# Kernel tuning notes

Hardware: AMD Instinct MI355X
Metric: run time of the kernel (lower is better)

The kernel has to match this reference:

```python
import jax, jax.numpy as jnp
import numpy as np

B, N, DIN, DOUT, DOP = 64, 512, 256, 256, 64
LN_EPS = 1e-5
NEG_SLOPE = 0.2


def setup_inputs() -> dict:
    key = jax.random.key(0)
    ks = jax.random.split(key, 16)
    stdv = 1.0 / np.sqrt(DOUT)

    def lin(k, shape, fan_in):
        # torch nn.Linear default init: U(-1/sqrt(fan_in), 1/sqrt(fan_in))
        bound = 1.0 / np.sqrt(fan_in)
        return jax.random.uniform(k, shape, jnp.float32, -bound, bound)

    return {
        "inputs": jax.random.normal(ks[0], (B, N, DIN), jnp.float32),
        "adj": jax.random.uniform(ks[1], (B, N, N), jnp.float32),
        "op_emb": jax.random.normal(ks[2], (B, N, DOP), jnp.float32),
        # DenseGraphFlow params
        "dgf_W": jax.random.uniform(ks[3], (DIN, DOUT), jnp.float32, -stdv, stdv),
        "dgf_b": jax.random.uniform(ks[4], (DOUT,), jnp.float32, -stdv, stdv),
        "dgf_opW": lin(ks[5], (DOUT, DOP), DOP),
        "dgf_opb": lin(ks[6], (DOUT,), DOP),
        # GraphAttentionLayer params
        "Wk": lin(ks[7], (DOUT, DIN), DIN),
        "Wv": lin(ks[8], (DOUT, DIN), DIN),
        "Wq": lin(ks[9], (DOUT, DIN), DIN),
        "a_w": lin(ks[10], (DOUT,), DOUT),
        "gat_opW": lin(ks[11], (DOUT, DOP), DOP),
        "gat_opb": lin(ks[12], (DOUT,), DOP),
        "ln_g": jnp.ones((DOUT,), jnp.float32),
        "ln_b": jnp.zeros((DOUT,), jnp.float32),
    }


def reference(inputs, adj, op_emb, dgf_W, dgf_b, dgf_opW, dgf_opb,
              Wk, Wv, Wq, a_w, gat_opW, gat_opb, ln_g, ln_b):
    # ----- DenseGraphFlow branch -----
    support = jnp.einsum('bni,io->bno', inputs, dgf_W)            # [B,N,DOUT]
    gate_d = jax.nn.sigmoid(op_emb @ dgf_opW.T + dgf_opb)        # [B,N,DOUT]
    dense = gate_d * jnp.einsum('bij,bjo->bio', adj, support)
    dense = dense + support + dgf_b                               # residual + bias

    # ----- GraphAttentionLayer branch -----
    Whk = inputs @ Wk.T                                           # [B,N,DOUT]
    Whv = inputs @ Wv.T
    Whq = inputs @ Wq.T
    # torch einsum 'balm,beam->belm' (a=1) builds Whq[b,e,:]*Whk[b,l,:];
    # a(.) contracts the feature dim -> equivalent fused score:
    scores = jnp.einsum('bem,blm,m->bel', Whq, Whk, a_w)
    scores = scores / jnp.sqrt(jnp.float32(DOUT))                 # attention_rescale
    alpha = jax.nn.leaky_relu(scores, NEG_SLOPE) * adj            # mask by multiply
    attn = jax.nn.softmax(alpha, axis=-1)                         # softmax over l (neighbors)
    gate_g = jax.nn.sigmoid(op_emb @ gat_opW.T + gat_opb)
    h_prime = gate_g * jnp.einsum('bel,blm->bem', attn, Whv)
    # LayerNorm over last dim
    mu = jnp.mean(h_prime, axis=-1, keepdims=True)
    var = jnp.var(h_prime, axis=-1, keepdims=True)
    gat = (h_prime - mu) * jax.lax.rsqrt(var + LN_EPS) * ln_g + ln_b

    return (dense + gat) * 0.5
```

## Files before the change

kernel.cpp:

```cpp
#include <hip/hip_runtime.h>
#include <cstdint>
#include <cstddef>

typedef unsigned short u16;
typedef unsigned int   u32;
typedef __attribute__((ext_vector_type(8))) short bf16x8;
typedef __attribute__((ext_vector_type(4))) float f32x4;

#define MFMA16(a,b,c) __builtin_amdgcn_mfma_f32_16x16x32_bf16((a),(b),(c),0,0,0)

__device__ __forceinline__ float bf2f(u16 h){
  union { u32 u; float f; } v; v.u = ((u32)h) << 16; return v.f;
}
__device__ __forceinline__ u16 f2bf(float f){
  union { float f; u32 u; } v; v.f = f;
  u32 u = v.u + 0x7FFFu + ((v.u >> 16) & 1u);
  return (u16)(u >> 16);
}
__device__ __forceinline__ float ldf(const void* p, int i, u32 isf32){
  return isf32 ? ((const float*)p)[i] : bf2f(((const u16*)p)[i]);
}
__device__ __forceinline__ void gld16(const u16* g, u16* l){
  __builtin_amdgcn_global_load_lds(
      (const __attribute__((address_space(1))) void*)g,
      (__attribute__((address_space(3))) void*)l, 16, 0, 0);
}

__global__ void kD_detect(const u16* __restrict__ raw, u32* __restrict__ flag)
{
  const int lane = threadIdx.x & 63;
  const float v = bf2f(raw[lane]);
  const unsigned long long big = __ballot(fabsf(v) > 1.0e6f);
  if (lane == 0) flag[0] = (big != 0ull) ? 1u : 0u;
}

__global__ void kC_conv(const void* __restrict__ src, u16* __restrict__ dst,
                        int n, const u32* __restrict__ flag)
{
  const int i8 = (blockIdx.x * 256 + threadIdx.x) << 3;
  if (i8 >= n) return;
  if (flag[0]) {
    const float4 a = ((const float4*)src)[i8 >> 2];
    const float4 b = ((const float4*)src)[(i8 >> 2) + 1];
    u16 o[8] = { f2bf(a.x), f2bf(a.y), f2bf(a.z), f2bf(a.w),
                 f2bf(b.x), f2bf(b.y), f2bf(b.z), f2bf(b.w) };
    *(uint4*)&dst[i8] = *(const uint4*)o;
  } else {
    ((uint4*)dst)[i8 >> 3] = ((const uint4*)src)[i8 >> 3];
  }
}

__global__ void kP_params(const void* dgf_opW, const void* gat_opW,
                          const void* dgf_b,   const void* dgf_opb,
                          const void* gat_opb, const void* ln_g,
                          const void* ln_b,    u16* __restrict__ PB,
                          const u32* __restrict__ flag)
{
  const int i = blockIdx.x * 256 + threadIdx.x;
  if (i >= 34048) return;
  const u32 f = flag[0];
  float v;
  if      (i < 16384) v = ldf(dgf_opW, i, f);
  else if (i < 32768) v = ldf(gat_opW, i - 16384, f);
  else if (i < 33024) v = ldf(dgf_b,   i - 32768, f);
  else if (i < 33280) v = ldf(dgf_opb, i - 33024, f);
  else if (i < 33536) v = ldf(gat_opb, i - 33280, f);
  else if (i < 33792) v = ldf(ln_g,    i - 33536, f);
  else                v = ldf(ln_b,    i - 33792, f);
  PB[i] = f2bf(v);
}

__global__ void k0_wcat(const void* dgfW, const void* Wk, const void* Wv,
                        const void* Wq, const void* aw, u16* __restrict__ Wcat,
                        const u32* __restrict__ flag)
{
  const int o = blockIdx.x;
  const int i = threadIdx.x;
  const u32 f = flag[0];
  float v;
  if (o < 256)       v = ldf(dgfW, i * 256 + o, f);
  else if (o < 512)  v = ldf(Wk, (o - 256) * 256 + i, f);
  else if (o < 768)  v = ldf(Wv, (o - 512) * 256 + i, f);
  else               v = ldf(Wq, (o - 768) * 256 + i, f) * ldf(aw, o - 768, f) * 0.0625f;
  Wcat[o * 256 + i] = f2bf(v);
}

__global__ __launch_bounds__(256, 2)
void k1_proj(const u16* __restrict__ X, const u16* __restrict__ W,
             u16* __restrict__ P, u16* __restrict__ T)
{
  __shared__ __align__(16) u16 ldsA[128 * 64];
  __shared__ __align__(16) u16 ldsB[128 * 64];
  const int bt = blockIdx.x;
  const int ct = blockIdx.y;
  const int r0 = bt << 7;
  const bool swapped = (ct == 4) | (ct == 5) | (ct >= 8);
  const int wbase = (ct < 8) ? (ct << 7) : ((ct - 8) << 7);
  const int tid = threadIdx.x;
  const int wave = tid >> 6;
  const int lane = tid & 63;
  const int wm = wave >> 1, wn = wave & 1;

  int gA[4], gB[4], dS[4];
#pragma unroll
  for (int s = 0; s < 4; ++s) {
    const int slot = ((wave * 4 + s) << 6) + lane;
    const int m = slot >> 3, c = slot & 7;
    const int kb = c ^ (m & 7);
    gA[s] = (r0 + m) * 256 + (kb << 3);
    gB[s] = (wbase + m) * 256 + (kb << 3);
    dS[s] = slot << 3;
  }

  f32x4 acc[4][4];
#pragma unroll
  for (int i = 0; i < 4; ++i)
#pragma unroll
    for (int j = 0; j < 4; ++j) acc[i][j] = f32x4{0.f, 0.f, 0.f, 0.f};

  for (int kt = 0; kt < 4; ++kt) {
    __syncthreads();
#pragma unroll
    for (int s = 0; s < 4; ++s) {
      gld16(X + gA[s] + (kt << 6), &ldsA[dS[s]]);
      gld16(W + gB[s] + (kt << 6), &ldsB[dS[s]]);
    }
    __syncthreads();
#pragma unroll
    for (int ks = 0; ks < 2; ++ks) {
      const int kb = (ks << 2) + (lane >> 4);
      bf16x8 fa[4], fb[4];
#pragma unroll
      for (int i = 0; i < 4; ++i) {
        const int m = (wm << 6) + (i << 4) + (lane & 15);
        fa[i] = *(const bf16x8*)&ldsA[((m << 3) + (kb ^ (m & 7))) << 3];
        const int n = (wn << 6) + (i << 4) + (lane & 15);
        fb[i] = *(const bf16x8*)&ldsB[((n << 3) + (kb ^ (n & 7))) << 3];
      }
      if (!swapped) {
#pragma unroll
        for (int i = 0; i < 4; ++i)
#pragma unroll
          for (int j = 0; j < 4; ++j)
            acc[i][j] = MFMA16(fa[i], fb[j], acc[i][j]);
      } else {
#pragma unroll
        for (int i = 0; i < 4; ++i)
#pragma unroll
          for (int j = 0; j < 4; ++j)
            acc[i][j] = MFMA16(fb[i], fa[j], acc[i][j]);
      }
    }
  }

  if (!swapped) {
    const int pcb = (ct < 4) ? (ct << 7) : ((ct - 2) << 7);
#pragma unroll
    for (int i = 0; i < 4; ++i) {
      const int row = r0 + (wm << 6) + (i << 4) + ((lane >> 4) << 2);
#pragma unroll
      for (int j = 0; j < 4; ++j) {
        const int col = pcb + (wn << 6) + (j << 4) + (lane & 15);
#pragma unroll
        for (int r = 0; r < 4; ++r)
          P[(row + r) * 768 + col] = f2bf(acc[i][j][r]);
      }
    }
  } else {
    const int trb = (wbase >= 512) ? (wbase - 256) : wbase;
    const int b = r0 >> 9;
    const int e0 = r0 & 511;
    u16* Tb = T + ((size_t)b << 18);
#pragma unroll
    for (int i = 0; i < 4; ++i) {
      const int trow = trb + (wn << 6) + (i << 4) + ((lane >> 4) << 2);
#pragma unroll
      for (int j = 0; j < 4; ++j) {
        const int e = e0 + (wm << 6) + (j << 4) + (lane & 15);
#pragma unroll
        for (int r = 0; r < 4; ++r)
          Tb[((trow + r) << 9) + e] = f2bf(acc[i][j][r]);
      }
    }
  }
}

__global__ __launch_bounds__(256, 2)
void k2_gates(const u16* __restrict__ OP, const u16* __restrict__ PB,
              u16* __restrict__ G)
{
  __shared__ __align__(16) u16 ldsA[128 * 64];
  __shared__ __align__(16) u16 ldsB[128 * 64];
  const int bt = blockIdx.x, ct = blockIdx.y;
  const int r0 = bt << 7;
  const u16* Wp = (ct < 2) ? (PB + (ct << 7) * 64) : (PB + 16384 + ((ct - 2) << 7) * 64);
  const u16* Bp = (ct < 2) ? (PB + 33024 + (ct << 7)) : (PB + 33280 + ((ct - 2) << 7));
  const int tid = threadIdx.x, wave = tid >> 6, lane = tid & 63;
  const int wm = wave >> 1, wn = wave & 1;

  f32x4 acc[4][4];
#pragma unroll
  for (int i = 0; i < 4; ++i)
#pragma unroll
    for (int j = 0; j < 4; ++j) acc[i][j] = f32x4{0.f, 0.f, 0.f, 0.f};

#pragma unroll
  for (int s = 0; s < 4; ++s) {
    const int slot = ((wave * 4 + s) << 6) + lane;
    const int m = slot >> 3, c = slot & 7;
    const int kb = c ^ (m & 7);
    *(uint4*)&ldsA[slot << 3] = *(const uint4*)(OP + (r0 + m) * 64 + (kb << 3));
    *(uint4*)&ldsB[slot << 3] = *(const uint4*)(Wp + m * 64 + (kb << 3));
  }
  __syncthreads();
#pragma unroll
  for (int ks = 0; ks < 2; ++ks) {
    const int kb = (ks << 2) + (lane >> 4);
    bf16x8 fa[4], fb[4];
#pragma unroll
    for (int i = 0; i < 4; ++i) {
      const int m = (wm << 6) + (i << 4) + (lane & 15);
      fa[i] = *(const bf16x8*)&ldsA[((m << 3) + (kb ^ (m & 7))) << 3];
      const int n = (wn << 6) + (i << 4) + (lane & 15);
      fb[i] = *(const bf16x8*)&ldsB[((n << 3) + (kb ^ (n & 7))) << 3];
    }
#pragma unroll
    for (int i = 0; i < 4; ++i)
#pragma unroll
      for (int j = 0; j < 4; ++j)
        acc[i][j] = MFMA16(fa[i], fb[j], acc[i][j]);
  }
#pragma unroll
  for (int i = 0; i < 4; ++i) {
    const int row = r0 + (wm << 6) + (i << 4) + ((lane >> 4) << 2);
#pragma unroll
    for (int j = 0; j < 4; ++j) {
      const int cw = (wn << 6) + (j << 4) + (lane & 15);
      const float bias = bf2f(Bp[cw]);
      const int col = (ct << 7) + cw;
#pragma unroll
      for (int r = 0; r < 4; ++r) {
        const float x = acc[i][j][r] + bias;
        G[((row + r) << 9) + col] = f2bf(1.0f / (1.0f + __expf(-x)));
      }
    }
  }
}

__global__ __launch_bounds__(256, 2)
void k3_scores(const u16* __restrict__ P, const u16* __restrict__ adj,
               u16* __restrict__ E)
{
  __shared__ __align__(16) u16 ldsA[128 * 64];
  __shared__ __align__(16) u16 ldsB[128 * 64];
  const int lt = blockIdx.x, et = blockIdx.y, b = blockIdx.z;
  const int e0 = et << 7, l0 = lt << 7;
  const int tid = threadIdx.x, wave = tid >> 6, lane = tid & 63;
  const int wm = wave >> 1, wn = wave & 1;
  const int rowQ = (b << 9) + e0;
  const int rowK = (b << 9) + l0;

  int gA[4], gB[4], dS[4];
#pragma unroll
  for (int s = 0; s < 4; ++s) {
    const int slot = ((wave * 4 + s) << 6) + lane;
    const int m = slot >> 3, c = slot & 7;
    const int kb = c ^ (m & 7);
    gA[s] = (rowQ + m) * 768 + 512 + (kb << 3);
    gB[s] = (rowK + m) * 768 + 256 + (kb << 3);
    dS[s] = slot << 3;
  }

  f32x4 acc[4][4];
#pragma unroll
  for (int i = 0; i < 4; ++i)
#pragma unroll
    for (int j = 0; j < 4; ++j) acc[i][j] = f32x4{0.f, 0.f, 0.f, 0.f};

  for (int kt = 0; kt < 4; ++kt) {
    __syncthreads();
#pragma unroll
    for (int s = 0; s < 4; ++s) {
      gld16(P + gA[s] + (kt << 6), &ldsA[dS[s]]);
      gld16(P + gB[s] + (kt << 6), &ldsB[dS[s]]);
    }
    __syncthreads();
#pragma unroll
    for (int ks = 0; ks < 2; ++ks) {
      const int kb = (ks << 2) + (lane >> 4);
      bf16x8 fa[4], fb[4];
#pragma unroll
      for (int i = 0; i < 4; ++i) {
        const int m = (wm << 6) + (i << 4) + (lane & 15);
        fa[i] = *(const bf16x8*)&ldsA[((m << 3) + (kb ^ (m & 7))) << 3];
        const int n = (wn << 6) + (i << 4) + (lane & 15);
        fb[i] = *(const bf16x8*)&ldsB[((n << 3) + (kb ^ (n & 7))) << 3];
      }
#pragma unroll
      for (int i = 0; i < 4; ++i)
#pragma unroll
        for (int j = 0; j < 4; ++j)
          acc[i][j] = MFMA16(fa[i], fb[j], acc[i][j]);
    }
  }
#pragma unroll
  for (int i = 0; i < 4; ++i) {
    const int e = e0 + (wm << 6) + (i << 4) + ((lane >> 4) << 2);
#pragma unroll
    for (int j = 0; j < 4; ++j) {
      const int l = l0 + (wn << 6) + (j << 4) + (lane & 15);
#pragma unroll
      for (int r = 0; r < 4; ++r) {
        const int idx = (((b << 9) + e + r) << 9) + l;
        const float a = bf2f(adj[idx]);
        float s = acc[i][j][r];
        s = (s > 0.0f ? s : 0.2f * s) * a;
        E[idx] = f2bf(__expf(s));
      }
    }
  }
}

__global__ __launch_bounds__(256, 2)
void k4_out(const u16* __restrict__ P, const u16* __restrict__ T,
            const u16* __restrict__ E, const u16* __restrict__ adj,
            const u16* __restrict__ G, const u16* __restrict__ PB,
            void* __restrict__ out, const u32* __restrict__ flag)
{
  __shared__ __align__(16) u16 ldsA[64 * 64];
  __shared__ __align__(16) u16 ldsB[256 * 64];
  __shared__ float red[64][4];
  const int et = blockIdx.x, b = blockIdx.y;
  const int e0 = et << 6;
  const int tid = threadIdx.x, wave = tid >> 6, lane = tid & 63;
  const int wm = wave >> 1, wn = wave & 1;
  const size_t abase = ((size_t)((b << 9) + e0)) << 9;
  const u16* Ea  = E + abase;
  const u16* Aa  = adj + abase;
  const u16* Tb  = T + ((size_t)b << 18);
  const u16* WhvT = Tb + (256 << 9);
  const u16* SupT = Tb;
  const u16* dgf_b = PB + 32768;
  const u16* ln_g  = PB + 33536;
  const u16* ln_b  = PB + 33792;
  const u32 isf32 = flag[0];

  int gA[2], dA[2], gB[8], dB[8];
#pragma unroll
  for (int s2 = 0; s2 < 2; ++s2) {
    const int slot = ((wave * 2 + s2) << 6) + lane;
    const int m = slot >> 3, c = slot & 7;
    gA[s2] = (m << 9) + ((c ^ (m & 7)) << 3);
    dA[s2] = slot << 3;
  }
#pragma unroll
  for (int s2 = 0; s2 < 8; ++s2) {
    const int slot = ((wave * 8 + s2) << 6) + lane;
    const int m = slot >> 3, c = slot & 7;
    gB[s2] = (m << 9) + ((c ^ (m & 7)) << 3);
    dB[s2] = slot << 3;
  }

  f32x4 acc[2][2][8], accS[2];
#pragma unroll
  for (int i = 0; i < 2; ++i) {
    accS[i] = f32x4{0.f, 0.f, 0.f, 0.f};
#pragma unroll
    for (int p = 0; p < 2; ++p)
#pragma unroll
      for (int j = 0; j < 8; ++j) acc[p][i][j] = f32x4{0.f, 0.f, 0.f, 0.f};
  }
  const short onebf = (short)0x3F80;
  const bf16x8 ones = {onebf, onebf, onebf, onebf, onebf, onebf, onebf, onebf};

#pragma unroll
  for (int ph = 0; ph < 2; ++ph) {
    const u16* Ag = ph ? Aa : Ea;
    const u16* Bg = ph ? SupT : WhvT;
    for (int lt = 0; lt < 8; ++lt) {
      __syncthreads();
#pragma unroll
      for (int s2 = 0; s2 < 2; ++s2)
        gld16(Ag + gA[s2] + (lt << 6), &ldsA[dA[s2]]);
#pragma unroll
      for (int s2 = 0; s2 < 8; ++s2)
        gld16(Bg + gB[s2] + (lt << 6), &ldsB[dB[s2]]);
      __syncthreads();
#pragma unroll
      for (int ks = 0; ks < 2; ++ks) {
        const int kb = (ks << 2) + (lane >> 4);
        bf16x8 fa[2];
#pragma unroll
        for (int i = 0; i < 2; ++i) {
          const int m = (wm << 5) + (i << 4) + (lane & 15);
          fa[i] = *(const bf16x8*)&ldsA[((m << 3) + (kb ^ (m & 7))) << 3];
        }
#pragma unroll
        for (int j = 0; j < 8; ++j) {
          const int n = (wn << 7) + (j << 4) + (lane & 15);
          const bf16x8 fb = *(const bf16x8*)&ldsB[((n << 3) + (kb ^ (n & 7))) << 3];
          acc[ph][0][j] = MFMA16(fa[0], fb, acc[ph][0][j]);
          acc[ph][1][j] = MFMA16(fa[1], fb, acc[ph][1][j]);
        }
        if (ph == 0) {
          accS[0] = MFMA16(fa[0], ones, accS[0]);
          accS[1] = MFMA16(fa[1], ones, accS[1]);
        }
      }
    }
  }

  const int cb = wn << 7;
  float lng[8], lnb[8], dgb[8];
#pragma unroll
  for (int j = 0; j < 8; ++j) {
    const int col = cb + (j << 4) + (lane & 15);
    lng[j] = bf2f(ln_g[col]);
    lnb[j] = bf2f(ln_b[col]);
    dgb[j] = bf2f(dgf_b[col]);
  }
#pragma unroll
  for (int i = 0; i < 2; ++i) {
#pragma unroll
    for (int r = 0; r < 4; ++r) {
      const int rl = (wm << 5) + (i << 4) + ((lane >> 4) << 2) + r;
      const int grow = (b << 9) + e0 + rl;
      const float invS = 1.0f / accS[i][r];
      float ps = 0.0f, pq = 0.0f;
#pragma unroll
      for (int j = 0; j < 8; ++j) {
        const int col = cb + (j << 4) + (lane & 15);
        const float gg = bf2f(G[((size_t)grow << 9) + 256 + col]);
        const float hp = gg * acc[0][i][j][r] * invS;
        acc[0][i][j][r] = hp;
        ps += hp; pq += hp * hp;
      }
#pragma unroll
      for (int m = 1; m < 16; m <<= 1) {
        ps += __shfl_xor(ps, m, 64);
        pq += __shfl_xor(pq, m, 64);
      }
      if ((lane & 15) == 0) { red[rl][wn << 1] = ps; red[rl][(wn << 1) + 1] = pq; }
    }
  }
  __syncthreads();
#pragma unroll
  for (int i = 0; i < 2; ++i) {
#pragma unroll
    for (int r = 0; r < 4; ++r) {
      const int rl = (wm << 5) + (i << 4) + ((lane >> 4) << 2) + r;
      const int grow = (b << 9) + e0 + rl;
      const float mean = (red[rl][0] + red[rl][2]) * (1.0f / 256.0f);
      const float ex2  = (red[rl][1] + red[rl][3]) * (1.0f / 256.0f);
      const float rstd = rsqrtf(ex2 - mean * mean + 1e-5f);
#pragma unroll
      for (int j = 0; j < 8; ++j) {
        const int col = cb + (j << 4) + (lane & 15);
        const float gat = (acc[0][i][j][r] - mean) * rstd * lng[j] + lnb[j];
        const float gd = bf2f(G[((size_t)grow << 9) + col]);
        const float sup = bf2f(P[grow * 768 + col]);
        const float dense = gd * acc[1][i][j][r] + sup + dgb[j];
        const float o = 0.5f * (dense + gat);
        if (isf32) ((float*)out)[grow * 256 + col] = o;
        else       ((u16*)out)[grow * 256 + col] = f2bf(o);
      }
    }
  }
}

extern "C" void kernel_launch(void* const* d_in, const int* in_sizes, int n_in,
                              void* d_out, int out_size, void* d_ws, size_t ws_size,
                              hipStream_t stream)
{
  (void)in_sizes; (void)n_in; (void)out_size; (void)ws_size;
  const void* inputs  = d_in[0];
  const void* adj     = d_in[1];
  const void* op_emb  = d_in[2];
  const void* dgf_W   = d_in[3];
  const void* dgf_b   = d_in[4];
  const void* dgf_opW = d_in[5];
  const void* dgf_opb = d_in[6];
  const void* Wk      = d_in[7];
  const void* Wv      = d_in[8];
  const void* Wq      = d_in[9];
  const void* a_w     = d_in[10];
  const void* gat_opW = d_in[11];
  const void* gat_opb = d_in[12];
  const void* ln_g    = d_in[13];
  const void* ln_b    = d_in[14];
  char* ws = (char*)d_ws;

  u16*  P    = (u16*)(ws);
  u16*  T    = (u16*)(ws + 50331648ull);
  u16*  E    = (u16*)(ws + 83886080ull);
  u16*  G    = (u16*)(ws + 117440512ull);
  u16*  Cadj = (u16*)(ws + 150994944ull);
  u16*  Cin  = (u16*)(ws + 184549376ull);
  u16*  Cop  = (u16*)(ws + 201326592ull);
  u16*  Wcat = (u16*)(ws + 205520896ull);
  u16*  PB   = (u16*)(ws + 206045184ull);
  u32*  flag = (u32*)(ws + 206245888ull);

  kD_detect <<<dim3(1),       dim3(64),  0, stream>>>((const u16*)inputs, flag);
  kC_conv   <<<dim3(4096),    dim3(256), 0, stream>>>(inputs, Cin,  8388608, flag);
  kC_conv   <<<dim3(1024),    dim3(256), 0, stream>>>(op_emb, Cop,  2097152, flag);
  kC_conv   <<<dim3(8192),    dim3(256), 0, stream>>>(adj,    Cadj, 16777216, flag);
  kP_params <<<dim3(134),     dim3(256), 0, stream>>>(dgf_opW, gat_opW, dgf_b,
                                                      dgf_opb, gat_opb, ln_g, ln_b,
                                                      PB, flag);
  k0_wcat   <<<dim3(1024),    dim3(256), 0, stream>>>(dgf_W, Wk, Wv, Wq, a_w,
                                                      Wcat, flag);
  k1_proj   <<<dim3(256, 10), dim3(256), 0, stream>>>(Cin, Wcat, P, T);
  k2_gates  <<<dim3(256, 4),  dim3(256), 0, stream>>>(Cop, PB, G);
  k3_scores <<<dim3(4, 4, 64),dim3(256), 0, stream>>>(P, Cadj, E);
  k4_out    <<<dim3(8, 64),   dim3(256), 0, stream>>>(P, T, E, Cadj, G,
                                                      PB, d_out, flag);
}
```

Measured before the change: 323.5 us.

## Split k4_out across 8 waves and raise occupancy bounds on GEMM kernels

k4_out now runs 512 threads (8 waves, 2x4 wave grid), so each wave owns 64 output columns instead of 128, which halves the per-wave accumulator registers. Its tile loads switch from direct global-to-LDS loads to register-staged uint4 loads that are issued before the first barrier, so global latency can overlap the wait. k1_proj and k3_scores request 4 blocks per CU instead of 2, which may force register spilling in exchange for more resident waves. The LayerNorm reduction buffer grows to combine partial sums from four column waves.

```diff
diff --git a/kernel.cpp b/kernel.cpp
--- a/kernel.cpp
+++ b/kernel.cpp
@@ -85,7 +85,7 @@
   Wcat[o * 256 + i] = f2bf(v);
 }
 
-__global__ __launch_bounds__(256, 2)
+__global__ __launch_bounds__(256, 4)
 void k1_proj(const u16* __restrict__ X, const u16* __restrict__ W,
              u16* __restrict__ P, u16* __restrict__ T)
 {
@@ -247,7 +247,7 @@
   }
 }
 
-__global__ __launch_bounds__(256, 2)
+__global__ __launch_bounds__(256, 4)
 void k3_scores(const u16* __restrict__ P, const u16* __restrict__ adj,
                u16* __restrict__ E)
 {
@@ -321,7 +321,7 @@
   }
 }
 
-__global__ __launch_bounds__(256, 2)
+__global__ __launch_bounds__(512, 4)
 void k4_out(const u16* __restrict__ P, const u16* __restrict__ T,
             const u16* __restrict__ E, const u16* __restrict__ adj,
             const u16* __restrict__ G, const u16* __restrict__ PB,
@@ -329,11 +329,11 @@
 {
   __shared__ __align__(16) u16 ldsA[64 * 64];
   __shared__ __align__(16) u16 ldsB[256 * 64];
-  __shared__ float red[64][4];
+  __shared__ float red[64][8];
   const int et = blockIdx.x, b = blockIdx.y;
   const int e0 = et << 6;
   const int tid = threadIdx.x, wave = tid >> 6, lane = tid & 63;
-  const int wm = wave >> 1, wn = wave & 1;
+  const int wm = wave >> 2, wn = wave & 3;
   const size_t abase = ((size_t)((b << 9) + e0)) << 9;
   const u16* Ea  = E + abase;
   const u16* Aa  = adj + abase;
@@ -345,30 +345,26 @@
   const u16* ln_b  = PB + 33792;
   const u32 isf32 = flag[0];
 
-  int gA[2], dA[2], gB[8], dB[8];
-#pragma unroll
-  for (int s2 = 0; s2 < 2; ++s2) {
-    const int slot = ((wave * 2 + s2) << 6) + lane;
+  const int am = tid >> 3, ac = tid & 7;
+  const int gAo = (am << 9) + ((ac ^ (am & 7)) << 3);
+  const int dAo = tid << 3;
+  int gBo[4], dBo[4];
+#pragma unroll
+  for (int q = 0; q < 4; ++q) {
+    const int slot = (q << 9) + tid;
     const int m = slot >> 3, c = slot & 7;
-    gA[s2] = (m << 9) + ((c ^ (m & 7)) << 3);
-    dA[s2] = slot << 3;
-  }
-#pragma unroll
-  for (int s2 = 0; s2 < 8; ++s2) {
-    const int slot = ((wave * 8 + s2) << 6) + lane;
-    const int m = slot >> 3, c = slot & 7;
-    gB[s2] = (m << 9) + ((c ^ (m & 7)) << 3);
-    dB[s2] = slot << 3;
-  }
-
-  f32x4 acc[2][2][8], accS[2];
+    gBo[q] = (m << 9) + ((c ^ (m & 7)) << 3);
+    dBo[q] = slot << 3;
+  }
+
+  f32x4 acc[2][2][4], accS[2];
 #pragma unroll
   for (int i = 0; i < 2; ++i) {
     accS[i] = f32x4{0.f, 0.f, 0.f, 0.f};
 #pragma unroll
     for (int p = 0; p < 2; ++p)
 #pragma unroll
-      for (int j = 0; j < 8; ++j) acc[p][i][j] = f32x4{0.f, 0.f, 0.f, 0.f};
+      for (int j = 0; j < 4; ++j) acc[p][i][j] = f32x4{0.f, 0.f, 0.f, 0.f};
   }
   const short onebf = (short)0x3F80;
   const bf16x8 ones = {onebf, onebf, onebf, onebf, onebf, onebf, onebf, onebf};
@@ -378,13 +374,15 @@
     const u16* Ag = ph ? Aa : Ea;
     const u16* Bg = ph ? SupT : WhvT;
     for (int lt = 0; lt < 8; ++lt) {
+      const uint4 ta = *(const uint4*)(Ag + gAo + (lt << 6));
+      uint4 tb[4];
+#pragma unroll
+      for (int q = 0; q < 4; ++q)
+        tb[q] = *(const uint4*)(Bg + gBo[q] + (lt << 6));
       __syncthreads();
-#pragma unroll
-      for (int s2 = 0; s2 < 2; ++s2)
-        gld16(Ag + gA[s2] + (lt << 6), &ldsA[dA[s2]]);
-#pragma unroll
-      for (int s2 = 0; s2 < 8; ++s2)
-        gld16(Bg + gB[s2] + (lt << 6), &ldsB[dB[s2]]);
+      *(uint4*)&ldsA[dAo] = ta;
+#pragma unroll
+      for (int q = 0; q < 4; ++q) *(uint4*)&ldsB[dBo[q]] = tb[q];
       __syncthreads();
 #pragma unroll
       for (int ks = 0; ks < 2; ++ks) {
@@ -396,8 +394,8 @@
           fa[i] = *(const bf16x8*)&ldsA[((m << 3) + (kb ^ (m & 7))) << 3];
         }
 #pragma unroll
-        for (int j = 0; j < 8; ++j) {
-          const int n = (wn << 7) + (j << 4) + (lane & 15);
+        for (int j = 0; j < 4; ++j) {
+          const int n = (wn << 6) + (j << 4) + (lane & 15);
           const bf16x8 fb = *(const bf16x8*)&ldsB[((n << 3) + (kb ^ (n & 7))) << 3];
           acc[ph][0][j] = MFMA16(fa[0], fb, acc[ph][0][j]);
           acc[ph][1][j] = MFMA16(fa[1], fb, acc[ph][1][j]);
@@ -410,10 +408,10 @@
     }
   }
 
-  const int cb = wn << 7;
-  float lng[8], lnb[8], dgb[8];
-#pragma unroll
-  for (int j = 0; j < 8; ++j) {
+  const int cb = wn << 6;
+  float lng[4], lnb[4], dgb[4];
+#pragma unroll
+  for (int j = 0; j < 4; ++j) {
     const int col = cb + (j << 4) + (lane & 15);
     lng[j] = bf2f(ln_g[col]);
     lnb[j] = bf2f(ln_b[col]);
@@ -428,7 +426,7 @@
       const float invS = 1.0f / accS[i][r];
       float ps = 0.0f, pq = 0.0f;
 #pragma unroll
-      for (int j = 0; j < 8; ++j) {
+      for (int j = 0; j < 4; ++j) {
         const int col = cb + (j << 4) + (lane & 15);
         const float gg = bf2f(G[((size_t)grow << 9) + 256 + col]);
         const float hp = gg * acc[0][i][j][r] * invS;
@@ -450,11 +448,11 @@
     for (int r = 0; r < 4; ++r) {
       const int rl = (wm << 5) + (i << 4) + ((lane >> 4) << 2) + r;
       const int grow = (b << 9) + e0 + rl;
-      const float mean = (red[rl][0] + red[rl][2]) * (1.0f / 256.0f);
-      const float ex2  = (red[rl][1] + red[rl][3]) * (1.0f / 256.0f);
+      const float mean = (red[rl][0] + red[rl][2] + red[rl][4] + red[rl][6]) * (1.0f / 256.0f);
+      const float ex2  = (red[rl][1] + red[rl][3] + red[rl][5] + red[rl][7]) * (1.0f / 256.0f);
       const float rstd = rsqrtf(ex2 - mean * mean + 1e-5f);
 #pragma unroll
-      for (int j = 0; j < 8; ++j) {
+      for (int j = 0; j < 4; ++j) {
         const int col = cb + (j << 4) + (lane & 15);
         const float gat = (acc[0][i][j][r] - mean) * rstd * lng[j] + lnb[j];
         const float gd = bf2f(G[((size_t)grow << 9) + col]);
@@ -513,6 +511,6 @@
   k1_proj   <<<dim3(256, 10), dim3(256), 0, stream>>>(Cin, Wcat, P, T);
   k2_gates  <<<dim3(256, 4),  dim3(256), 0, stream>>>(Cop, PB, G);
   k3_scores <<<dim3(4, 4, 64),dim3(256), 0, stream>>>(P, Cadj, E);
-  k4_out    <<<dim3(8, 64),   dim3(256), 0, stream>>>(P, T, E, Cadj, G,
+  k4_out    <<<dim3(8, 64),   dim3(512), 0, stream>>>(P, T, E, Cadj, G,
                                                       PB, d_out, flag);
 }
```

After: 572.6 us. 77.0% more time.
